# Kernel optimization log

Hardware: AMD Instinct MI355X
Metric: run time of the kernel (lower is better)

Reference implementation:

```python
import jax, jax.numpy as jnp
import numpy as np

B0, K, H, W = 8, 1, 512, 512
S, CS, NMS, M = 25, 51, 5, 2048
REG_W, COV_POW = 1.0, 0.5

def _gauss_kernel(n):
    x = jnp.linspace(-1.0, 1.0, n)
    g = jnp.exp(-x * x / 0.5)
    return g / g.sum()

def _conv1d2d(x, k1d, horizontal, pad_h, pad_w):
    # x: [B,1,H,W]; replicates torch F.conv2d with the given (possibly asymmetric) padding
    kern = k1d.reshape(1, 1, 1, -1) if horizontal else k1d.reshape(1, 1, -1, 1)
    return jax.lax.conv_general_dilated(x, kern, (1, 1), [(pad_h, pad_h), (pad_w, pad_w)],
                                        dimension_numbers=("NCHW", "OIHW", "NCHW"))

def bilinear_sample(img, pts):
    # img [B,C,H,W], pts [B,N,2] (x,y in [-1,1]); grid_sample bilinear, align_corners=False, zero padding
    Bb, C, Hh, Ww = img.shape
    x = (pts[..., 0] + 1.0) * 0.5 * Ww - 0.5
    y = (pts[..., 1] + 1.0) * 0.5 * Hh - 0.5
    x0 = jnp.floor(x); y0 = jnp.floor(y)
    wx = x - x0; wy = y - y0
    x0i = x0.astype(jnp.int32); y0i = y0.astype(jnp.int32)
    flat = img.reshape(Bb, C, Hh * Ww)
    def tap(yi, xi, w):
        ok = ((yi >= 0) & (yi < Hh) & (xi >= 0) & (xi < Ww)).astype(img.dtype)
        idx = jnp.clip(yi, 0, Hh - 1) * Ww + jnp.clip(xi, 0, Ww - 1)  # [B,N]
        v = jnp.take_along_axis(flat, idx[:, None, :], axis=2)        # [B,C,N]
        return v * (w * ok)[:, None, :]
    return (tap(y0i, x0i, (1 - wy) * (1 - wx)) + tap(y0i, x0i + 1, (1 - wy) * wx)
            + tap(y0i + 1, x0i, wy * (1 - wx)) + tap(y0i + 1, x0i + 1, wy * wx))

def compute_matchability(keypoint_p, has_depth, Bt):
    G = _gauss_kernel(S)
    # NOTE: faithful to original asymmetric padding bug: pad H while convolving along W, then pad W while convolving along H
    s = _conv1d2d(keypoint_p.reshape(Bt, 1, H, W), G, True, S // 2, 0)
    s = _conv1d2d(s, G, False, 0, S // 2)
    log_p_hat = jax.nn.log_softmax(jnp.log(s.reshape(Bt, H * W) + 1e-8), axis=-1)
    sd = _conv1d2d(has_depth.reshape(Bt, 1, H, W), G, True, 0, S // 2)
    sd = _conv1d2d(sd, G, False, S // 2, 0).reshape(Bt, H * W)
    p = sd / sd.sum(-1, keepdims=True)
    return jnp.sum(jnp.where(p > 0, p * (jnp.log(jnp.maximum(p, 1e-30)) - log_p_hat), 0.0), axis=-1)

def sample_keypoints(sm):
    # sm [B,H,W]; coverage-reweighted NMS + top-k (topk=True, subpixel=False)
    wcov = jnp.exp(-jnp.square(jnp.linspace(-2.0, 2.0, CS)))
    ld = _conv1d2d(((sm + 1e-6) * 1e4)[:, None], wcov, True, 0, CS // 2)
    ld = _conv1d2d(ld, wcov, False, CS // 2, 0)[:, 0]
    sm = sm * (ld + 1e-8) ** (-COV_POW)
    p = NMS // 2
    mx = jax.lax.reduce_window(sm, -jnp.inf, jax.lax.max, (1, NMS, NMS), (1, 1, 1),
                               [(0, 0), (p, p), (p, p)])
    sm = sm * (sm == mx)
    _, inds = jax.lax.top_k(sm.reshape(-1, H * W), M)
    xs = (jnp.arange(W) + 0.5) * 2.0 / W - 1.0
    ys = (jnp.arange(H) + 0.5) * 2.0 / H - 1.0
    grid = jnp.stack(jnp.meshgrid(xs, ys, indexing="xy"), axis=-1).reshape(H * W, 2)
    return jnp.take(grid, inds, axis=0)  # [B,M,2] normalized (x,y)

def masked_log_softmax(logits, mask):
    return jax.nn.log_softmax(jnp.where(mask, logits, -1e9), axis=-1)

def _reward(d):
    return jnp.exp(-100.0 * d)

def _forward(scoremap, gt_warp_A2B, gt_warp_B2A, valid_A2B, valid_B2A, has_depth):
    sg = jax.lax.stop_gradient
    lA = scoremap[:B0].reshape(B0, K, H * W)
    lB = scoremap[B0:].reshape(B0, K, H * W)
    logits = jnp.concatenate([lA, lB], 0)                                   # [2B,K,HW]
    kp_p = jax.nn.softmax(logits.reshape(2 * B0, K * H * W), -1).reshape(2 * B0, K, H * W).sum(1)
    match_loss = compute_matchability(kp_p, sg(has_depth), 2 * B0).mean()
    # sparse branch is under torch.set_grad_enabled(False)
    kpts_A = sample_keypoints(sg(kp_p[:B0]).reshape(B0, H, W))
    kpts_B = sample_keypoints(sg(kp_p[B0:]).reshape(B0, H, W))
    kpts_A2B = bilinear_sample(sg(gt_warp_A2B[..., 2:]).transpose(0, 3, 1, 2), kpts_A).transpose(0, 2, 1)
    kpts_B2A = bilinear_sample(sg(gt_warp_B2A[..., 2:]).transpose(0, 3, 1, 2), kpts_B).transpose(0, 2, 1)
    legit_A2B = bilinear_sample(sg(valid_A2B)[:, None], kpts_A)[:, 0] > 0   # [B,M]
    legit_B2A = bilinear_sample(sg(valid_B2A)[:, None], kpts_B)[:, 0] > 0
    dA = jnp.sqrt(jnp.sum(jnp.square(kpts_A2B[:, :, None] - kpts_B[:, None]), -1) + 1e-12).min(-1)
    dB = jnp.sqrt(jnp.sum(jnp.square(kpts_B2A[:, :, None] - kpts_A[:, None]), -1) + 1e-12).min(-1)
    rA = _reward(dA); rB = _reward(dB)
    slA = bilinear_sample(lA.reshape(B0, 1, H, W), kpts_A)[:, 0]            # [B,M]
    slB = bilinear_sample(lB.reshape(B0, 1, H, W), kpts_B)[:, 0]
    lpA = masked_log_softmax(slA, legit_A2B)
    lpB = masked_log_softmax(slB, legit_B2A)
    sparse = -jnp.sum(jnp.where(legit_A2B, rA * lpA, 0.0)) - jnp.sum(jnp.where(legit_B2A, rB * lpB, 0.0))
    return sparse + REG_W * match_loss

def setup_inputs() -> dict:
    key = jax.random.key(0)
    ks = jax.random.split(key, 6)
    scoremap = jax.random.normal(ks[0], (2 * B0, K, H, W), jnp.float32)
    gt_warp_A2B = jax.random.uniform(ks[1], (B0, H, W, 4), jnp.float32, -1.0, 1.0)
    gt_warp_B2A = jax.random.uniform(ks[2], (B0, H, W, 4), jnp.float32, -1.0, 1.0)
    valid_A2B = (jax.random.uniform(ks[3], (B0, H, W)) > 0.3).astype(jnp.float32)
    valid_B2A = (jax.random.uniform(ks[4], (B0, H, W)) > 0.3).astype(jnp.float32)
    has_depth = (jax.random.uniform(ks[5], (2 * B0, H, W)) > 0.3).astype(jnp.float32)
    return dict(scoremap=scoremap, gt_warp_A2B=gt_warp_A2B, gt_warp_B2A=gt_warp_B2A,
                valid_A2B=valid_A2B, valid_B2A=valid_B2A, has_depth=has_depth)

def reference(scoremap, gt_warp_A2B, gt_warp_B2A, valid_A2B, valid_B2A, has_depth):
    return _forward(scoremap, gt_warp_A2B, gt_warp_B2A, valid_A2B, valid_B2A, has_depth)
```

## Files before the change

kernel.cpp:

```cpp
#include <hip/hip_runtime.h>

#define HH 512
#define WW 512
#define HW_ 262144
#define NIMG 16
#define MK 2048
#define CAPB 4096
#define SCAP 32768
#define SBUFN 768

static constexpr size_t OFF_B1    = 16777216;
static constexpr size_t OFF_B2    = 33554432;
static constexpr size_t OFF_SMALL = 50331648;
static constexpr size_t OFF_SEL  = 4194304;
static constexpr size_t OFF_BND  = 4325376;
static constexpr size_t OFF_PP   = 4849664;
static constexpr size_t OFF_WXp  = 5111808;
static constexpr size_t OFF_WYp  = 5242880;
static constexpr size_t OFF_LG   = 5373952;
static constexpr size_t OFF_SL   = 5505024;
static constexpr size_t OFF_PMIN = 5636096;
static constexpr size_t OFF_HIST = 33554432;
static constexpr size_t OFF_SURV = 33554432 + 4194304;

#define CSTRIDE 32

__device__ __forceinline__ float wred64(float v) {
  for (int m = 1; m < 64; m <<= 1) v += __shfl_xor(v, m);
  return v;
}

__device__ __forceinline__ void g25_wave0(float* g) {
  int t = threadIdx.x;
  if (t < 64) {
    float raw = 0.0f;
    if (t < 25) {
      float x = -1.0f + (float)t * (2.0f / 24.0f);
      raw = expf(-(x * x) / 0.5f);
    }
    float s = raw;
    for (int m = 1; m < 64; m <<= 1) s += __shfl_xor(s, m);
    if (t < 25) g[t] = raw / s;
  }
}
__device__ __forceinline__ void w51_wave0(float* wc) {
  int t = threadIdx.x;
  if (t < 51) {
    float x = -2.0f + (float)t * (4.0f / 50.0f);
    wc[t] = expf(-x * x);
  }
}

template<int B>
__device__ __forceinline__ float brsum(float v, float* red) {
  int t = threadIdx.x;
  red[t] = v; __syncthreads();
  for (int s = B >> 1; s > 0; s >>= 1) {
    if (t < s) red[t] += red[t + s];
    __syncthreads();
  }
  float r = red[0]; __syncthreads();
  return r;
}
template<int B>
__device__ __forceinline__ float brmax(float v, float* red) {
  int t = threadIdx.x;
  red[t] = v; __syncthreads();
  for (int s = B >> 1; s > 0; s >>= 1) {
    if (t < s) red[t] = fmaxf(red[t], red[t + s]);
    __syncthreads();
  }
  float r = red[0]; __syncthreads();
  return r;
}

__global__ void __launch_bounds__(256)
k_pre(const float* __restrict__ x, const float* __restrict__ hd, float* A,
      float* sume, float* sumS, float* Zb) {
  __shared__ float g[25];
  __shared__ float red[12];
  int tid = threadIdx.x;
  g25_wave0(g);
  size_t base = (size_t)blockIdx.x * 1024;
  size_t e = base + tid * 4;
  float4 xs = *(const float4*)(x + e);
  float4 hs = *(const float4*)(hd + e);
  __syncthreads();
  int rem = (int)(e & (HW_ - 1));
  int y = rem >> 9, x0 = rem & 511;
  float wv = 0.0f;
  {
    int k0 = y - 499; if (k0 < 0) k0 = 0;
    int k1 = y + 12;  if (k1 > 24) k1 = 24;
    for (int k = k0; k <= k1; k++) wv += g[k];
  }
  float cwv[4], cpv[4];
  {
    int lo = x0 - 487; if (lo < 0) lo = 0;
    int hi = x0;       if (hi > 24) hi = 24;
    float c = 0.0f;
    for (int d = lo; d <= hi; d++) c += g[d];
    cwv[0] = c;
    for (int q = 1; q < 4; q++) {
      int i = x0 + q;
      if (i <= 24) c += g[i];
      if (i >= 488) c -= g[i - 488];
      cwv[q] = c;
    }
  }
  {
    int lo = x0 - 499; if (lo < 0) lo = 0;
    int hi = x0 + 12;  if (hi > 24) hi = 24;
    float c = 0.0f;
    for (int d = lo; d <= hi; d++) c += g[d];
    cpv[0] = c;
    for (int q = 1; q < 4; q++) {
      int i = x0 + q;
      if (i + 12 <= 24) c += g[i + 12];
      if (i >= 500) c -= g[i - 500];
      cpv[q] = c;
    }
  }
  float e0 = expf(xs.x), e1 = expf(xs.y), e2 = expf(xs.z), e3 = expf(xs.w);
  *(float4*)(A + e) = make_float4(e0, e1, e2, e3);
  float r0 = (e0 + e1) + (e2 + e3);
  float r1 = (e0 * cwv[0] + e1 * cwv[1] + e2 * cwv[2] + e3 * cwv[3]) * wv;
  float r2 = (hs.x * cpv[0] + hs.y * cpv[1] + hs.z * cpv[2] + hs.w * cpv[3]) * wv;
  r0 = wred64(r0); r1 = wred64(r1); r2 = wred64(r2);
  int wid = tid >> 6;
  if ((tid & 63) == 0) { red[wid] = r0; red[4 + wid] = r1; red[8 + wid] = r2; }
  __syncthreads();
  if (tid == 0) {
    int img = (int)(base >> 18);
    atomicAdd(&sume[img * CSTRIDE], red[0] + red[1] + red[2] + red[3]);
    atomicAdd(&sumS[img * CSTRIDE], red[4] + red[5] + red[6] + red[7]);
    atomicAdd(&Zb[img * CSTRIDE], red[8] + red[9] + red[10] + red[11]);
  }
}

__global__ void __launch_bounds__(256)
k_hconv(const float* __restrict__ A, const float* __restrict__ hd,
        const float* __restrict__ sume, float* b1, float* b2) {
  __shared__ __align__(16) float ta[512];
  __shared__ __align__(16) float th[536];
  __shared__ float g[25];
  int tid = threadIdx.x;
  int blk = blockIdx.x;
  int img = blk >> 9;
  size_t rowoff = (size_t)blk * 512;
  g25_wave0(g);
  ((float2*)ta)[tid] = *(const float2*)(A + rowoff + tid * 2);
  ((float2*)(th + 12))[tid] = *(const float2*)(hd + rowoff + tid * 2);
  if (tid < 12) { th[tid] = 0.0f; th[524 + tid] = 0.0f; }
  __syncthreads();
  float inv = 1.0f / sume[img * CSTRIDE];
  int j = 2 * tid;
  float v1a = 0.0f, v1b = 0.0f;
  if (tid >= 6 && tid <= 249) {
    float w[26];
#pragma unroll
    for (int d = 0; d < 26; d++) w[d] = ta[j - 12 + d];
#pragma unroll
    for (int d = 0; d < 25; d++) {
      v1a = fmaf(g[d], w[d], v1a);
      v1b = fmaf(g[d], w[d + 1], v1b);
    }
  }
  float v2a = 0.0f, v2b = 0.0f;
  {
    float u[26];
#pragma unroll
    for (int d = 0; d < 26; d++) u[d] = th[j + d];
#pragma unroll
    for (int d = 0; d < 25; d++) {
      v2a = fmaf(g[d], u[d], v2a);
      v2b = fmaf(g[d], u[d + 1], v2b);
    }
  }
  ((float2*)b1)[blk * 256 + tid] = make_float2(v1a * inv, v1b * inv);
  ((float2*)b2)[blk * 256 + tid] = make_float2(v2a, v2b);
}

__global__ void __launch_bounds__(256)
k_match(const float* __restrict__ b1, const float* __restrict__ b2,
        const float* __restrict__ sume, const float* sumS, const float* Zb,
        float* macc) {
  __shared__ float g[25];
  __shared__ float t1[88 * 64];
  __shared__ float t2[88 * 64];
  __shared__ float red4[4];
  g25_wave0(g);
  int blk = blockIdx.x;
  int img = blk >> 6;
  int ty = (blk >> 3) & 7;
  int tx = blk & 7;
  int y0 = ty * 64, x0 = tx * 64;
  const float* base1 = b1 + (size_t)img * HW_;
  const float* base2 = b2 + (size_t)img * HW_;
  for (int i = threadIdx.x; i < 88 * 64; i += 256) {
    int r = i >> 6, c = i & 63;
    int y = y0 + r - 12;
    float v1 = 0.0f, v2 = 0.0f;
    if (y >= 0 && y < 512) {
      size_t o = (size_t)y * 512 + x0 + c;
      v1 = base1[o]; v2 = base2[o];
    }
    t1[i] = v1; t2[i] = v2;
  }
  __syncthreads();
  float Z = Zb[img * CSTRIDE];
  float inv = 1.0f / sume[img * CSTRIDE];
  float logS = logf(sumS[img * CSTRIDE] * inv + (float)HW_ * 1e-8f);
  float acc = 0.0f;
  for (int w = threadIdx.x; w < 1024; w += 256) {
    int rg = w >> 6, c = w & 63;
    int r0 = rg * 4;
    float s[4] = {0.f, 0.f, 0.f, 0.f};
    float d[4] = {0.f, 0.f, 0.f, 0.f};
#pragma unroll
    for (int i = 0; i < 28; i++) {
      float v1 = t1[(r0 + i) * 64 + c];
      float v2 = t2[(r0 + i) * 64 + c];
#pragma unroll
      for (int jj = 0; jj < 4; jj++) {
        if (i >= jj && i - jj < 25) {
          s[jj] = fmaf(g[i - jj], v1, s[jj]);
          d[jj] = fmaf(g[i - jj], v2, d[jj]);
        }
      }
    }
#pragma unroll
    for (int jj = 0; jj < 4; jj++) {
      float p = d[jj] / Z;
      if (p > 0.0f)
        acc += p * (logf(fmaxf(p, 1e-30f)) - (logf(s[jj] + 1e-8f) - logS));
    }
  }
  acc = wred64(acc);
  if ((threadIdx.x & 63) == 0) red4[threadIdx.x >> 6] = acc;
  __syncthreads();
  if (threadIdx.x == 0)
    atomicAdd(macc, red4[0] + red4[1] + red4[2] + red4[3]);
}

__global__ void __launch_bounds__(256)
k_h51(const float* __restrict__ A, const float* __restrict__ sume, float* out) {
  __shared__ float wc[51];
  __shared__ __align__(16) float ta[564];
  int tid = threadIdx.x;
  int blk = blockIdx.x;
  int img = blk >> 9;
  size_t rowoff = (size_t)blk * 512;
  w51_wave0(wc);
  float s1 = 1e4f / sume[img * CSTRIDE];
  for (int i = tid; i < 562; i += 256) {
    int j = i - 25;
    ta[i] = ((unsigned)j < 512u) ? fmaf(A[rowoff + j], s1, 1e-2f) : 0.0f;
  }
  __syncthreads();
  int j = 2 * tid;
  float w[52];
#pragma unroll
  for (int d = 0; d < 52; d++) w[d] = ta[j + d];
  float va = 0.0f, vb = 0.0f;
#pragma unroll
  for (int d = 0; d < 51; d++) {
    va = fmaf(wc[d], w[d], va);
    vb = fmaf(wc[d], w[d + 1], vb);
  }
  ((float2*)out)[blk * 256 + tid] = make_float2(va, vb);
}

__global__ void __launch_bounds__(512, 6)
k_smwnms(const float* __restrict__ A, const float* __restrict__ sume,
         const float* __restrict__ b1,
         unsigned long long* surv, unsigned* scnt, unsigned* hist) {
  __shared__ float wc[53];
  __shared__ __align__(16) float tb1[119 * 68];
  __shared__ __align__(16) float tsm[68 * 68];
  __shared__ unsigned lcnt;
  __shared__ unsigned gbase;
  float* hm = tb1;
  unsigned long long* sbuf = (unsigned long long*)(tb1 + 4352);
  int tid = threadIdx.x;
  w51_wave0(wc);
  if (tid == 51 || tid == 52) wc[tid] = 0.0f;
  if (tid == 0) lcnt = 0;
  int blk = blockIdx.x;
  int img = blk >> 6;
  int ty = (blk >> 3) & 7;
  int tx = blk & 7;
  int y0 = ty * 64, x0 = tx * 64;
  const float* base = b1 + (size_t)img * HW_;
  for (int i = tid; i < 119 * 34; i += 512) {
    int r = i / 34, c2 = i - r * 34;
    int y = y0 + r - 27;
    int x = x0 + c2 * 2 - 2;
    float2 v = make_float2(0.0f, 0.0f);
    if ((unsigned)y < 512u && (unsigned)x < 512u)
      v = *(const float2*)(base + (size_t)y * 512 + x);
    *(float2*)(tb1 + r * 68 + c2 * 2) = v;
  }
  __syncthreads();
  float inv = 1.0f / sume[img * CSTRIDE];
  const float* abase = A + (size_t)img * HW_;
  if (tid < 23 * 17) {
    int rg = tid / 17, cg = tid - rg * 17;
    int r0 = rg * 3, c0 = cg * 4;
    int nr = (r0 <= 65) ? 3 : 2;
    float a0x = 0.f, a0y = 0.f, a0z = 0.f, a0w = 0.f;
    float a1x = 0.f, a1y = 0.f, a1z = 0.f, a1w = 0.f;
    float a2x = 0.f, a2y = 0.f, a2z = 0.f, a2w = 0.f;
    float w1 = 0.f, w2 = 0.f;
    const float* tp = tb1 + r0 * 68 + c0;
#pragma unroll 4
    for (int i = 0; i < 53; i++) {
      float4 v = *(const float4*)(tp + i * 68);
      float w0 = wc[i];
      a0x = fmaf(w0, v.x, a0x); a0y = fmaf(w0, v.y, a0y);
      a0z = fmaf(w0, v.z, a0z); a0w = fmaf(w0, v.w, a0w);
      a1x = fmaf(w1, v.x, a1x); a1y = fmaf(w1, v.y, a1y);
      a1z = fmaf(w1, v.z, a1z); a1w = fmaf(w1, v.w, a1w);
      a2x = fmaf(w2, v.x, a2x); a2y = fmaf(w2, v.y, a2y);
      a2z = fmaf(w2, v.z, a2z); a2w = fmaf(w2, v.w, a2w);
      w2 = w1; w1 = w0;
    }
    auto storerow = [&](int jj, float ax, float ay, float az, float aw) {
      int r = r0 + jj;
      int y = y0 + r - 2;
      int xb = x0 + c0 - 2;
      float4 res = make_float4(-3.4e38f, -3.4e38f, -3.4e38f, -3.4e38f);
      if ((unsigned)y < 512u) {
        const float* ar = abase + (size_t)y * 512;
        if ((unsigned)xb < 512u) {
          float2 p = *(const float2*)(ar + xb);
          res.x = (p.x * inv) / sqrtf(ax + 1e-8f);
          res.y = (p.y * inv) / sqrtf(ay + 1e-8f);
        }
        if ((unsigned)(xb + 2) < 512u) {
          float2 p = *(const float2*)(ar + xb + 2);
          res.z = (p.x * inv) / sqrtf(az + 1e-8f);
          res.w = (p.y * inv) / sqrtf(aw + 1e-8f);
        }
      }
      *(float4*)(tsm + r * 68 + c0) = res;
    };
    storerow(0, a0x, a0y, a0z, a0w);
    storerow(1, a1x, a1y, a1z, a1w);
    if (nr == 3) storerow(2, a2x, a2y, a2z, a2w);
  }
  __syncthreads();
  for (int i = tid; i < 68 * 16; i += 512) {
    int r = i >> 4, cg = i & 15;
    const float* row = tsm + r * 68 + cg * 4;
    float4 v0 = *(const float4*)(row);
    float4 v1 = *(const float4*)(row + 4);
    float p01 = fmaxf(v0.x, v0.y), p12 = fmaxf(v0.y, v0.z);
    float p23 = fmaxf(v0.z, v0.w), p34 = fmaxf(v0.w, v1.x);
    float p45 = fmaxf(v1.x, v1.y), p56 = fmaxf(v1.y, v1.z);
    float m0 = fmaxf(fmaxf(p01, p23), v1.x);
    float m1 = fmaxf(fmaxf(p12, p34), v1.y);
    float m2 = fmaxf(fmaxf(p23, p45), v1.z);
    float m3 = fmaxf(fmaxf(p34, p56), v1.w);
    *(float4*)(hm + r * 64 + cg * 4) = make_float4(m0, m1, m2, m3);
  }
  __syncthreads();
  for (int k0 = 0; k0 < 2; k0++) {
    int i = tid + k0 * 512;
    int r = i >> 4, cb = (i & 15) * 4;
    const float* tp2 = tsm + (r + 2) * 68 + cb + 2;
    float2 va = *(const float2*)(tp2);
    float2 vb = *(const float2*)(tp2 + 2);
    float4 m0 = *(const float4*)(hm + r * 64 + cb);
    float4 m1 = *(const float4*)(hm + (r + 1) * 64 + cb);
    float4 m2 = *(const float4*)(hm + (r + 2) * 64 + cb);
    float4 m3 = *(const float4*)(hm + (r + 3) * 64 + cb);
    float4 m4 = *(const float4*)(hm + (r + 4) * 64 + cb);
    float Mx = fmaxf(fmaxf(m0.x, m1.x), fmaxf(fmaxf(m2.x, m3.x), m4.x));
    float My = fmaxf(fmaxf(m0.y, m1.y), fmaxf(fmaxf(m2.y, m3.y), m4.y));
    float Mz = fmaxf(fmaxf(m0.z, m1.z), fmaxf(fmaxf(m2.z, m3.z), m4.z));
    float Mw = fmaxf(fmaxf(m0.w, m1.w), fmaxf(fmaxf(m2.w, m3.w), m4.w));
    auto keepf = [&](float vk, float Mk, int k) {
      if (vk == Mk && vk != 0.0f) {
        unsigned p = atomicAdd(&lcnt, 1u);
        unsigned bits = __float_as_uint(vk);
        unsigned idx = (unsigned)((y0 + r) * 512 + x0 + cb + k);
        if (p < SBUFN)
          sbuf[p] = ((unsigned long long)bits << 32) |
                    (unsigned long long)(idx ^ 0xFFFFFFFFu);
        atomicAdd(&hist[(size_t)img * 65536 + (bits >> 16)], 1u);
      }
    };
    keepf(va.x, Mx, 0); keepf(va.y, My, 1);
    keepf(vb.x, Mz, 2); keepf(vb.y, Mw, 3);
  }
  __syncthreads();
  unsigned total = lcnt; if (total > SBUFN) total = SBUFN;
  if (tid == 0) gbase = atomicAdd(&scnt[img * CSTRIDE], total);
  __syncthreads();
  unsigned gb = gbase;
  for (unsigned i = tid; i < total; i += 512) {
    unsigned p = gb + i;
    if (p < SCAP) surv[(size_t)img * SCAP + p] = sbuf[i];
  }
}

__global__ void k_thresh(const unsigned* __restrict__ hist, unsigned* Tb, unsigned* needb) {
  int img = blockIdx.x;
  const unsigned* h = hist + (size_t)img * 65536;
  __shared__ unsigned part[256];
  __shared__ unsigned scan[257];
  int t = threadIdx.x;
  unsigned s = 0;
  for (int k = 0; k < 256; k++) {
    int bin = 65535 - (t * 256 + k);
    s += (bin == 0) ? 0x00100000u : h[bin];
  }
  part[t] = s; __syncthreads();
  if (t == 0) {
    unsigned c = 0;
    for (int k = 0; k < 256; k++) { scan[k] = c; c += part[k]; }
    scan[256] = c;
  }
  __syncthreads();
  unsigned pre = scan[t];
  if (pre < MK && pre + part[t] >= MK) {
    unsigned c = pre;
    for (int k = 0; k < 256; k++) {
      int bin = 65535 - (t * 256 + k);
      unsigned cnt = (bin == 0) ? 0x00100000u : h[bin];
      if (c + cnt >= MK) { Tb[img * CSTRIDE] = (unsigned)bin; needb[img * CSTRIDE] = MK - c; break; }
      c += cnt;
    }
  }
}

__global__ void k_collect(const unsigned long long* __restrict__ surv,
                          const unsigned* __restrict__ scnt,
                          const unsigned* __restrict__ Tb,
                          unsigned* selcnt, unsigned* sel,
                          unsigned* bcnt, unsigned long long* bnd) {
  int blk = blockIdx.x;
  int img = blk >> 7;
  int i = (blk & 127) * 256 + threadIdx.x;
  unsigned cnt = scnt[img * CSTRIDE]; if (cnt > SCAP) cnt = SCAP;
  unsigned long long entry = ((unsigned)i < cnt) ? surv[(size_t)img * SCAP + i] : 0ull;
  unsigned bits = (unsigned)(entry >> 32);
  unsigned bin = bits >> 16;
  unsigned T = Tb[img * CSTRIDE];
  bool ok = (unsigned)i < cnt;
  bool c1 = ok && (bin > T);
  bool c2 = ok && (bin == T);
  int lane = threadIdx.x & 63;
  unsigned long long lowmask = (1ull << lane) - 1ull;

  unsigned long long m1 = __ballot(c1);
  if (m1) {
    int leader = __ffsll(m1) - 1;
    unsigned base = 0;
    if (lane == leader) base = atomicAdd(&selcnt[img * CSTRIDE], (unsigned)__popcll(m1));
    base = __shfl(base, leader);
    if (c1) {
      unsigned p = base + (unsigned)__popcll(m1 & lowmask);
      if (p < MK) sel[img * MK + p] = (unsigned)(entry & 0xFFFFFFFFull) ^ 0xFFFFFFFFu;
    }
  }
  unsigned long long m2 = __ballot(c2);
  if (m2) {
    int leader = __ffsll(m2) - 1;
    unsigned base = 0;
    if (lane == leader) base = atomicAdd(&bcnt[img * CSTRIDE], (unsigned)__popcll(m2));
    base = __shfl(base, leader);
    if (c2) {
      unsigned p = base + (unsigned)__popcll(m2 & lowmask);
      if (p < CAPB) bnd[(size_t)img * CAPB + p] = entry;
    }
  }
}

__global__ void __launch_bounds__(1024)
k_finsel(const unsigned long long* __restrict__ bnd, const unsigned* bcnt,
         const unsigned* needb, const unsigned* selcnt, unsigned* sel) {
  int img = blockIdx.x;
  __shared__ unsigned long long key[CAPB];
  unsigned bn = bcnt[img * CSTRIDE];
  int n = (bn < CAPB) ? (int)bn : CAPB;
  int np2 = 2;
  while (np2 < n) np2 <<= 1;
  int t = threadIdx.x;
  for (int k = t; k < np2; k += 1024)
    key[k] = (k < n) ? bnd[(size_t)img * CAPB + k] : 0ull;
  __syncthreads();
  for (int sz = 2; sz <= np2; sz <<= 1) {
    for (int st = sz >> 1; st > 0; st >>= 1) {
      for (int i = t; i < np2; i += 1024) {
        int l = i ^ st;
        if (l > i) {
          unsigned long long a = key[i], b = key[l];
          bool up = ((i & sz) == 0);
          if (up ? (a < b) : (a > b)) { key[i] = b; key[l] = a; }
        }
      }
      __syncthreads();
    }
  }
  unsigned c1 = selcnt[img * CSTRIDE]; if (c1 > MK) c1 = MK;
  unsigned need = needb[img * CSTRIDE];
  unsigned kk = need; if (kk > MK - c1) kk = MK - c1;
  for (unsigned m = t; m < MK - c1; m += 1024) {
    unsigned v = 0u;
    if (m < kk && m < (unsigned)n)
      v = (unsigned)(key[m] & 0xFFFFFFFFull) ^ 0xFFFFFFFFu;
    sel[img * MK + c1 + m] = v;
  }
}

__global__ void k_prep(const unsigned* __restrict__ sel, const float* __restrict__ scoremap,
                       const float* __restrict__ gtA, const float* __restrict__ gtB,
                       const float* __restrict__ vA, const float* __restrict__ vB,
                       float2* pp, float* wx, float* wy, float* lg, float* sl) {
  int t = blockIdx.x * 256 + threadIdx.x;
  int img = t >> 11;
  unsigned idx = sel[t] & (HW_ - 1);
  int h = idx >> 9, w = idx & 511;
  pp[t] = make_float2((w + 0.5f) * (2.0f / 512.0f) - 1.0f,
                      (h + 0.5f) * (2.0f / 512.0f) - 1.0f);
  int b = (img < 8) ? img : img - 8;
  const float* gt = (img < 8) ? gtA : gtB;
  const float* vv = (img < 8) ? vA : vB;
  size_t pix = (size_t)b * HW_ + idx;
  float2 gxy = *(const float2*)(gt + pix * 4 + 2);
  wx[t] = gxy.x;
  wy[t] = gxy.y;
  lg[t] = (vv[pix] > 0.0f) ? 1.0f : 0.0f;
  sl[t] = scoremap[(size_t)img * HW_ + idx];
}

__global__ void __launch_bounds__(256)
k_mindist(const float2* __restrict__ pp,
          const float* __restrict__ wx, const float* __restrict__ wy,
          float* pmin) {
  __shared__ float2 opp[512];
  int blk = blockIdx.x;
  int img = blk >> 5;
  int qc = (blk >> 2) & 7;
  int oc = blk & 3;
  const float2* ob = pp + (size_t)(img ^ 8) * MK + oc * 512;
  for (int k = threadIdx.x; k < 512; k += 256) opp[k] = ob[k];
  __syncthreads();
  int m = img * MK + qc * 256 + threadIdx.x;
  float ax = wx[m], ay = wy[m];
  float d[8];
#pragma unroll
  for (int u = 0; u < 8; u++) d[u] = 3.4e38f;
  for (int n = 0; n < 512; n += 8) {
#pragma unroll
    for (int u = 0; u < 8; u++) {
      float2 o = opp[n + u];
      float dx = ax - o.x, dy = ay - o.y;
      d[u] = fminf(d[u], fmaf(dx, dx, dy * dy));
    }
  }
  float d2 = fminf(fminf(fminf(d[0], d[1]), fminf(d[2], d[3])),
                   fminf(fminf(d[4], d[5]), fminf(d[6], d[7])));
  pmin[oc * (NIMG * MK) + m] = d2;
}

__global__ void __launch_bounds__(1024)
k_loss(const float* __restrict__ sl, const float* __restrict__ lg,
       const float* __restrict__ pmin, float* sacc) {
  int img = blockIdx.x;
  __shared__ float red[1024];
  int t = threadIdx.x;
  int i0 = img * MK + t, i1 = i0 + 1024;
  float s0 = sl[i0], s1 = sl[i1];
  float g0 = lg[i0], g1 = lg[i1];
  float l0 = (g0 > 0.0f) ? s0 : -1e9f;
  float l1 = (g1 > 0.0f) ? s1 : -1e9f;
  float mx = brmax<1024>(fmaxf(l0, l1), red);
  float se = brsum<1024>(expf(l0 - mx) + expf(l1 - mx), red);
  float lse = mx + logf(se);
  const int ST = NIMG * MK;
  float a = 0.0f;
  if (g0 > 0.0f) {
    float mn = fminf(fminf(pmin[i0], pmin[ST + i0]),
                     fminf(pmin[2 * ST + i0], pmin[3 * ST + i0]));
    float r0 = expf(-100.0f * sqrtf(mn + 1e-12f));
    a += r0 * (s0 - lse);
  }
  if (g1 > 0.0f) {
    float mn = fminf(fminf(pmin[i1], pmin[ST + i1]),
                     fminf(pmin[2 * ST + i1], pmin[3 * ST + i1]));
    float r1 = expf(-100.0f * sqrtf(mn + 1e-12f));
    a += r1 * (s1 - lse);
  }
  float tot = brsum<1024>(a, red);
  if (t == 0) atomicAdd(sacc, -tot);
}

__global__ void k_out(const float* macc, const float* sacc, float* out) {
  out[0] = sacc[0] + macc[0] * (1.0f / 16.0f);
}

extern "C" void kernel_launch(void* const* d_in, const int* in_sizes, int n_in,
                              void* d_out, int out_size, void* d_ws, size_t ws_size,
                              hipStream_t stream) {
  const float* scoremap = (const float*)d_in[0];
  const float* gtA = (const float*)d_in[1];
  const float* gtB = (const float*)d_in[2];
  const float* vA  = (const float*)d_in[3];
  const float* vB  = (const float*)d_in[4];
  const float* hd  = (const float*)d_in[5];

  char* ws = (char*)d_ws;
  float* A  = (float*)(ws);
  float* B1 = (float*)(ws + OFF_B1);

  char* sm = ws + OFF_SMALL;
  float*    sume   = (float*)(sm + 0);
  float*    sumS   = (float*)(sm + 2048);
  float*    Zb     = (float*)(sm + 4096);
  unsigned* Tb     = (unsigned*)(sm + 6144);
  unsigned* needb  = (unsigned*)(sm + 8192);
  unsigned* selcnt = (unsigned*)(sm + 10240);
  unsigned* bcnt   = (unsigned*)(sm + 12288);
  float*    macc   = (float*)(sm + 14336);
  float*    sacc   = (float*)(sm + 14464);
  unsigned* scnt   = (unsigned*)(sm + 16384);

  unsigned* hist = (unsigned*)(ws + OFF_HIST);
  unsigned long long* surv = (unsigned long long*)(ws + OFF_SURV);
  unsigned* sel  = (unsigned*)(ws + OFF_SEL);
  unsigned long long* bnd = (unsigned long long*)(ws + OFF_BND);
  float2* pp = (float2*)(ws + OFF_PP);
  float* wx = (float*)(ws + OFF_WXp);
  float* wy = (float*)(ws + OFF_WYp);
  float* lg = (float*)(ws + OFF_LG);
  float* sl = (float*)(ws + OFF_SL);
  float* pmin = (float*)(ws + OFF_PMIN);
  float* B2 = (float*)(ws + 33554432);

  float* out = (float*)d_out;

  hipMemsetAsync(sm, 0, 32768, stream);

  k_pre<<<4096, 256, 0, stream>>>(scoremap, hd, A, sume, sumS, Zb);

  k_hconv<<<8192, 256, 0, stream>>>(A, hd, sume, B1, B2);
  k_match<<<1024, 256, 0, stream>>>(B1, B2, sume, sumS, Zb, macc);

  k_h51<<<8192, 256, 0, stream>>>(A, sume, B1);
  hipMemsetAsync(ws + OFF_HIST, 0, (size_t)16 * 65536 * 4, stream);

  k_smwnms<<<1024, 512, 0, stream>>>(A, sume, B1, surv, scnt, hist);
  k_thresh<<<16, 256, 0, stream>>>(hist, Tb, needb);
  k_collect<<<2048, 256, 0, stream>>>(surv, scnt, Tb, selcnt, sel, bcnt, bnd);
  k_finsel<<<16, 1024, 0, stream>>>(bnd, bcnt, needb, selcnt, sel);

  k_prep<<<128, 256, 0, stream>>>(sel, scoremap, gtA, gtB, vA, vB, pp, wx, wy, lg, sl);
  k_mindist<<<512, 256, 0, stream>>>(pp, wx, wy, pmin);
  k_loss<<<16, 1024, 0, stream>>>(sl, lg, pmin, sacc);
  k_out<<<1, 1, 0, stream>>>(macc, sacc, out);
}
```

Baseline: 318.0 us.

## Interleave conv buffers, fold memset and final kernel, parallelize threshold scan

Several unrelated changes land together. The weight sums in k_pre now come from a prefix table instead of loops. The two horizontal-conv outputs are interleaved into one buffer so k_match loads them with float4 and float2. The histogram zeroing moves into k_h51, replacing a memset. k_smwnms batches its tile loads and prefetches the A values early. k_thresh uses a 1024-thread vectorized wave-scan. k_out is merged into k_loss through a last-block counter. The aim is to cut launch count, memory passes and serial scan latency, at the cost of more complex code and an atomic completion protocol.

New measurement: 288.5 us. -9.3%, faster.

```diff
diff --git a/kernel.cpp b/kernel.cpp
--- a/kernel.cpp
+++ b/kernel.cpp
@@ -10,7 +10,6 @@
 #define SBUFN 768
 
 static constexpr size_t OFF_B1    = 16777216;
-static constexpr size_t OFF_B2    = 33554432;
 static constexpr size_t OFF_SMALL = 50331648;
 static constexpr size_t OFF_SEL  = 4194304;
 static constexpr size_t OFF_BND  = 4325376;
@@ -78,9 +77,15 @@
 k_pre(const float* __restrict__ x, const float* __restrict__ hd, float* A,
       float* sume, float* sumS, float* Zb) {
   __shared__ float g[25];
+  __shared__ float gp[26];
   __shared__ float red[12];
   int tid = threadIdx.x;
   g25_wave0(g);
+  if (tid == 0) {
+    float c = 0.0f;
+    gp[0] = 0.0f;
+    for (int k = 0; k < 25; k++) { c += g[k]; gp[k + 1] = c; }
+  }
   size_t base = (size_t)blockIdx.x * 1024;
   size_t e = base + tid * 4;
   float4 xs = *(const float4*)(x + e);
@@ -88,38 +93,22 @@
   __syncthreads();
   int rem = (int)(e & (HW_ - 1));
   int y = rem >> 9, x0 = rem & 511;
-  float wv = 0.0f;
+  float wv;
   {
     int k0 = y - 499; if (k0 < 0) k0 = 0;
     int k1 = y + 12;  if (k1 > 24) k1 = 24;
-    for (int k = k0; k <= k1; k++) wv += g[k];
+    wv = gp[k1 + 1] - gp[k0];
   }
   float cwv[4], cpv[4];
-  {
-    int lo = x0 - 487; if (lo < 0) lo = 0;
-    int hi = x0;       if (hi > 24) hi = 24;
-    float c = 0.0f;
-    for (int d = lo; d <= hi; d++) c += g[d];
-    cwv[0] = c;
-    for (int q = 1; q < 4; q++) {
-      int i = x0 + q;
-      if (i <= 24) c += g[i];
-      if (i >= 488) c -= g[i - 488];
-      cwv[q] = c;
-    }
-  }
-  {
-    int lo = x0 - 499; if (lo < 0) lo = 0;
-    int hi = x0 + 12;  if (hi > 24) hi = 24;
-    float c = 0.0f;
-    for (int d = lo; d <= hi; d++) c += g[d];
-    cpv[0] = c;
-    for (int q = 1; q < 4; q++) {
-      int i = x0 + q;
-      if (i + 12 <= 24) c += g[i + 12];
-      if (i >= 500) c -= g[i - 500];
-      cpv[q] = c;
-    }
+#pragma unroll
+  for (int q = 0; q < 4; q++) {
+    int i = x0 + q;
+    int lo = i - 487; if (lo < 0) lo = 0;
+    int hi = i;       if (hi > 24) hi = 24;
+    cwv[q] = gp[hi + 1] - gp[lo];
+    int lo2 = i - 499; if (lo2 < 0) lo2 = 0;
+    int hi2 = i + 12;  if (hi2 > 24) hi2 = 24;
+    cpv[q] = gp[hi2 + 1] - gp[lo2];
   }
   float e0 = expf(xs.x), e1 = expf(xs.y), e2 = expf(xs.z), e3 = expf(xs.w);
   *(float4*)(A + e) = make_float4(e0, e1, e2, e3);
@@ -140,7 +129,7 @@
 
 __global__ void __launch_bounds__(256)
 k_hconv(const float* __restrict__ A, const float* __restrict__ hd,
-        const float* __restrict__ sume, float* b1, float* b2) {
+        const float* __restrict__ sume, float* b12) {
   __shared__ __align__(16) float ta[512];
   __shared__ __align__(16) float th[536];
   __shared__ float g[25];
@@ -177,17 +166,16 @@
       v2b = fmaf(g[d], u[d + 1], v2b);
     }
   }
-  ((float2*)b1)[blk * 256 + tid] = make_float2(v1a * inv, v1b * inv);
-  ((float2*)b2)[blk * 256 + tid] = make_float2(v2a, v2b);
+  *(float4*)(b12 + (rowoff + j) * 2) =
+      make_float4(v1a * inv, v2a, v1b * inv, v2b);
 }
 
 __global__ void __launch_bounds__(256)
-k_match(const float* __restrict__ b1, const float* __restrict__ b2,
+k_match(const float* __restrict__ b12,
         const float* __restrict__ sume, const float* sumS, const float* Zb,
         float* macc) {
   __shared__ float g[25];
-  __shared__ float t1[88 * 64];
-  __shared__ float t2[88 * 64];
+  __shared__ __align__(16) float t12[88 * 128];
   __shared__ float red4[4];
   g25_wave0(g);
   int blk = blockIdx.x;
@@ -195,17 +183,16 @@
   int ty = (blk >> 3) & 7;
   int tx = blk & 7;
   int y0 = ty * 64, x0 = tx * 64;
-  const float* base1 = b1 + (size_t)img * HW_;
-  const float* base2 = b2 + (size_t)img * HW_;
-  for (int i = threadIdx.x; i < 88 * 64; i += 256) {
-    int r = i >> 6, c = i & 63;
+  const float* base12 = b12 + (size_t)img * HW_ * 2;
+  for (int i = threadIdx.x; i < 88 * 32; i += 256) {
+    int r = i >> 5, c4 = i & 31;
     int y = y0 + r - 12;
-    float v1 = 0.0f, v2 = 0.0f;
+    float4 v = make_float4(0.f, 0.f, 0.f, 0.f);
     if (y >= 0 && y < 512) {
-      size_t o = (size_t)y * 512 + x0 + c;
-      v1 = base1[o]; v2 = base2[o];
-    }
-    t1[i] = v1; t2[i] = v2;
+      size_t px = (size_t)y * 512 + x0 + c4 * 2;
+      v = *(const float4*)(base12 + px * 2);
+    }
+    *(float4*)(t12 + r * 128 + c4 * 4) = v;
   }
   __syncthreads();
   float Z = Zb[img * CSTRIDE];
@@ -219,13 +206,12 @@
     float d[4] = {0.f, 0.f, 0.f, 0.f};
 #pragma unroll
     for (int i = 0; i < 28; i++) {
-      float v1 = t1[(r0 + i) * 64 + c];
-      float v2 = t2[(r0 + i) * 64 + c];
+      float2 v = *(const float2*)(t12 + (r0 + i) * 128 + c * 2);
 #pragma unroll
       for (int jj = 0; jj < 4; jj++) {
         if (i >= jj && i - jj < 25) {
-          s[jj] = fmaf(g[i - jj], v1, s[jj]);
-          d[jj] = fmaf(g[i - jj], v2, d[jj]);
+          s[jj] = fmaf(g[i - jj], v.x, s[jj]);
+          d[jj] = fmaf(g[i - jj], v.y, d[jj]);
         }
       }
     }
@@ -244,7 +230,8 @@
 }
 
 __global__ void __launch_bounds__(256)
-k_h51(const float* __restrict__ A, const float* __restrict__ sume, float* out) {
+k_h51(const float* __restrict__ A, const float* __restrict__ sume, float* out,
+      unsigned* __restrict__ hist) {
   __shared__ float wc[51];
   __shared__ __align__(16) float ta[564];
   int tid = threadIdx.x;
@@ -252,6 +239,8 @@
   int img = blk >> 9;
   size_t rowoff = (size_t)blk * 512;
   w51_wave0(wc);
+  if (tid < 32)
+    ((uint4*)hist)[(size_t)blk * 32 + tid] = make_uint4(0u, 0u, 0u, 0u);
   float s1 = 1e4f / sume[img * CSTRIDE];
   for (int i = tid; i < 562; i += 256) {
     int j = i - 25;
@@ -292,14 +281,25 @@
   int tx = blk & 7;
   int y0 = ty * 64, x0 = tx * 64;
   const float* base = b1 + (size_t)img * HW_;
-  for (int i = tid; i < 119 * 34; i += 512) {
-    int r = i / 34, c2 = i - r * 34;
-    int y = y0 + r - 27;
-    int x = x0 + c2 * 2 - 2;
-    float2 v = make_float2(0.0f, 0.0f);
-    if ((unsigned)y < 512u && (unsigned)x < 512u)
-      v = *(const float2*)(base + (size_t)y * 512 + x);
-    *(float2*)(tb1 + r * 68 + c2 * 2) = v;
+  {
+    float2 vreg[8];
+    int laddr[8];
+#pragma unroll
+    for (int k = 0; k < 8; k++) {
+      int i = tid + k * 512;
+      bool ok = (i < 119 * 34);
+      int r = i / 34, c2 = i - r * 34;
+      int y = y0 + r - 27;
+      int x = x0 + c2 * 2 - 2;
+      float2 v = make_float2(0.0f, 0.0f);
+      if (ok && (unsigned)y < 512u && (unsigned)x < 512u)
+        v = *(const float2*)(base + (size_t)y * 512 + x);
+      vreg[k] = v;
+      laddr[k] = ok ? (r * 68 + c2 * 2) : -1;
+    }
+#pragma unroll
+    for (int k = 0; k < 8; k++)
+      if (laddr[k] >= 0) *(float2*)(tb1 + laddr[k]) = vreg[k];
   }
   __syncthreads();
   float inv = 1.0f / sume[img * CSTRIDE];
@@ -308,6 +308,19 @@
     int rg = tid / 17, cg = tid - rg * 17;
     int r0 = rg * 3, c0 = cg * 4;
     int nr = (r0 <= 65) ? 3 : 2;
+    float2 apre[3][2];
+#pragma unroll
+    for (int jj = 0; jj < 3; jj++) {
+      int y = y0 + r0 + jj - 2;
+      int xb = x0 + c0 - 2;
+      apre[jj][0] = make_float2(0.f, 0.f);
+      apre[jj][1] = make_float2(0.f, 0.f);
+      if ((unsigned)y < 512u) {
+        const float* ar = abase + (size_t)y * 512;
+        if ((unsigned)xb < 512u) apre[jj][0] = *(const float2*)(ar + xb);
+        if ((unsigned)(xb + 2) < 512u) apre[jj][1] = *(const float2*)(ar + xb + 2);
+      }
+    }
     float a0x = 0.f, a0y = 0.f, a0z = 0.f, a0w = 0.f;
     float a1x = 0.f, a1y = 0.f, a1z = 0.f, a1w = 0.f;
     float a2x = 0.f, a2y = 0.f, a2z = 0.f, a2w = 0.f;
@@ -325,29 +338,27 @@
       a2z = fmaf(w2, v.z, a2z); a2w = fmaf(w2, v.w, a2w);
       w2 = w1; w1 = w0;
     }
-    auto storerow = [&](int jj, float ax, float ay, float az, float aw) {
+    auto storerow = [&](int jj, float ax, float ay, float az, float aw,
+                        float2 p0, float2 p1) {
       int r = r0 + jj;
       int y = y0 + r - 2;
       int xb = x0 + c0 - 2;
       float4 res = make_float4(-3.4e38f, -3.4e38f, -3.4e38f, -3.4e38f);
       if ((unsigned)y < 512u) {
-        const float* ar = abase + (size_t)y * 512;
         if ((unsigned)xb < 512u) {
-          float2 p = *(const float2*)(ar + xb);
-          res.x = (p.x * inv) / sqrtf(ax + 1e-8f);
-          res.y = (p.y * inv) / sqrtf(ay + 1e-8f);
+          res.x = (p0.x * inv) / sqrtf(ax + 1e-8f);
+          res.y = (p0.y * inv) / sqrtf(ay + 1e-8f);
         }
         if ((unsigned)(xb + 2) < 512u) {
-          float2 p = *(const float2*)(ar + xb + 2);
-          res.z = (p.x * inv) / sqrtf(az + 1e-8f);
-          res.w = (p.y * inv) / sqrtf(aw + 1e-8f);
+          res.z = (p1.x * inv) / sqrtf(az + 1e-8f);
+          res.w = (p1.y * inv) / sqrtf(aw + 1e-8f);
         }
       }
       *(float4*)(tsm + r * 68 + c0) = res;
     };
-    storerow(0, a0x, a0y, a0z, a0w);
-    storerow(1, a1x, a1y, a1z, a1w);
-    if (nr == 3) storerow(2, a2x, a2y, a2z, a2w);
+    storerow(0, a0x, a0y, a0z, a0w, apre[0][0], apre[0][1]);
+    storerow(1, a1x, a1y, a1z, a1w, apre[1][0], apre[1][1]);
+    if (nr == 3) storerow(2, a2x, a2y, a2z, a2w, apre[2][0], apre[2][1]);
   }
   __syncthreads();
   for (int i = tid; i < 68 * 16; i += 512) {
@@ -405,29 +416,40 @@
   }
 }
 
-__global__ void k_thresh(const unsigned* __restrict__ hist, unsigned* Tb, unsigned* needb) {
+__global__ void __launch_bounds__(1024)
+k_thresh(const unsigned* __restrict__ hist, unsigned* Tb, unsigned* needb) {
   int img = blockIdx.x;
   const unsigned* h = hist + (size_t)img * 65536;
-  __shared__ unsigned part[256];
-  __shared__ unsigned scan[257];
+  __shared__ unsigned wsum[16];
+  __shared__ unsigned wpre[16];
   int t = threadIdx.x;
+  int b0 = 65472 - 64 * t;
+  const uint4* hv = (const uint4*)(h + b0);
   unsigned s = 0;
-  for (int k = 0; k < 256; k++) {
-    int bin = 65535 - (t * 256 + k);
-    s += (bin == 0) ? 0x00100000u : h[bin];
-  }
-  part[t] = s; __syncthreads();
-  if (t == 0) {
-    unsigned c = 0;
-    for (int k = 0; k < 256; k++) { scan[k] = c; c += part[k]; }
-    scan[256] = c;
-  }
-  __syncthreads();
-  unsigned pre = scan[t];
-  if (pre < MK && pre + part[t] >= MK) {
+#pragma unroll
+  for (int k = 0; k < 16; k++) {
+    uint4 u = hv[k];
+    s += u.x + u.y + u.z + u.w;
+  }
+  if (b0 == 0) s += 0x00100000u - h[0];
+  unsigned inc = s;
+  for (int m = 1; m < 64; m <<= 1) {
+    unsigned o = __shfl_up(inc, m);
+    if ((t & 63) >= m) inc += o;
+  }
+  if ((t & 63) == 63) wsum[t >> 6] = inc;
+  __syncthreads();
+  if (t < 16) {
+    unsigned p = 0;
+    for (int k = 0; k < 16; k++) if (k < t) p += wsum[k];
+    wpre[t] = p;
+  }
+  __syncthreads();
+  unsigned pre = wpre[t >> 6] + inc - s;
+  if (pre < MK && pre + s >= MK) {
     unsigned c = pre;
-    for (int k = 0; k < 256; k++) {
-      int bin = 65535 - (t * 256 + k);
+    for (int k = 0; k < 64; k++) {
+      int bin = 65535 - (t * 64 + k);
       unsigned cnt = (bin == 0) ? 0x00100000u : h[bin];
       if (c + cnt >= MK) { Tb[img * CSTRIDE] = (unsigned)bin; needb[img * CSTRIDE] = MK - c; break; }
       c += cnt;
@@ -568,7 +590,8 @@
 
 __global__ void __launch_bounds__(1024)
 k_loss(const float* __restrict__ sl, const float* __restrict__ lg,
-       const float* __restrict__ pmin, float* sacc) {
+       const float* __restrict__ pmin, float* sacc, float* macc, float* out,
+       unsigned* ldone) {
   int img = blockIdx.x;
   __shared__ float red[1024];
   int t = threadIdx.x;
@@ -595,11 +618,16 @@
     a += r1 * (s1 - lse);
   }
   float tot = brsum<1024>(a, red);
-  if (t == 0) atomicAdd(sacc, -tot);
-}
-
-__global__ void k_out(const float* macc, const float* sacc, float* out) {
-  out[0] = sacc[0] + macc[0] * (1.0f / 16.0f);
+  if (t == 0) {
+    atomicAdd(sacc, -tot);
+    __threadfence();
+    unsigned dnum = atomicAdd(ldone, 1u);
+    if (dnum == NIMG - 1) {
+      float sv = atomicAdd(sacc, 0.0f);
+      float mv = atomicAdd(macc, 0.0f);
+      out[0] = sv + mv * (1.0f / 16.0f);
+    }
+  }
 }
 
 extern "C" void kernel_launch(void* const* d_in, const int* in_sizes, int n_in,
@@ -613,8 +641,9 @@
   const float* hd  = (const float*)d_in[5];
 
   char* ws = (char*)d_ws;
-  float* A  = (float*)(ws);
-  float* B1 = (float*)(ws + OFF_B1);
+  float* A   = (float*)(ws);
+  float* B12 = (float*)(ws + OFF_B1);
+  float* B1p = (float*)(ws + OFF_B1);
 
   char* sm = ws + OFF_SMALL;
   float*    sume   = (float*)(sm + 0);
@@ -627,6 +656,7 @@
   float*    macc   = (float*)(sm + 14336);
   float*    sacc   = (float*)(sm + 14464);
   unsigned* scnt   = (unsigned*)(sm + 16384);
+  unsigned* ldone  = (unsigned*)(sm + 20480);
 
   unsigned* hist = (unsigned*)(ws + OFF_HIST);
   unsigned long long* surv = (unsigned long long*)(ws + OFF_SURV);
@@ -638,7 +668,6 @@
   float* lg = (float*)(ws + OFF_LG);
   float* sl = (float*)(ws + OFF_SL);
   float* pmin = (float*)(ws + OFF_PMIN);
-  float* B2 = (float*)(ws + 33554432);
 
   float* out = (float*)d_out;
 
@@ -646,19 +675,17 @@
 
   k_pre<<<4096, 256, 0, stream>>>(scoremap, hd, A, sume, sumS, Zb);
 
-  k_hconv<<<8192, 256, 0, stream>>>(A, hd, sume, B1, B2);
-  k_match<<<1024, 256, 0, stream>>>(B1, B2, sume, sumS, Zb, macc);
-
-  k_h51<<<8192, 256, 0, stream>>>(A, sume, B1);
-  hipMemsetAsync(ws + OFF_HIST, 0, (size_t)16 * 65536 * 4, stream);
-
-  k_smwnms<<<1024, 512, 0, stream>>>(A, sume, B1, surv, scnt, hist);
-  k_thresh<<<16, 256, 0, stream>>>(hist, Tb, needb);
+  k_hconv<<<8192, 256, 0, stream>>>(A, hd, sume, B12);
+  k_match<<<1024, 256, 0, stream>>>(B12, sume, sumS, Zb, macc);
+
+  k_h51<<<8192, 256, 0, stream>>>(A, sume, B1p, hist);
+
+  k_smwnms<<<1024, 512, 0, stream>>>(A, sume, B1p, surv, scnt, hist);
+  k_thresh<<<16, 1024, 0, stream>>>(hist, Tb, needb);
   k_collect<<<2048, 256, 0, stream>>>(surv, scnt, Tb, selcnt, sel, bcnt, bnd);
   k_finsel<<<16, 1024, 0, stream>>>(bnd, bcnt, needb, selcnt, sel);
 
   k_prep<<<128, 256, 0, stream>>>(sel, scoremap, gtA, gtB, vA, vB, pp, wx, wy, lg, sl);
   k_mindist<<<512, 256, 0, stream>>>(pp, wx, wy, pmin);
-  k_loss<<<16, 1024, 0, stream>>>(sl, lg, pmin, sacc);
-  k_out<<<1, 1, 0, stream>>>(macc, sacc, out);
-}
+  k_loss<<<16, 1024, 0, stream>>>(sl, lg, pmin, sacc, macc, out, ldone);
+}
```
